# Kernel optimization log

Hardware: AMD Instinct MI355X
Metric: run time of the kernel (lower is better)

The kernel has to match this reference:

```python
import jax, jax.numpy as jnp
import numpy as np

D_MODEL = 1024
D_STATE = 16
DT_RANK = 64  # ceil(1024/16)
DT_MIN, DT_MAX = 1e-3, 1e-1


def setup_inputs() -> dict:
    key = jax.random.key(0)
    ks = jax.random.split(key, 6)
    x = jax.random.normal(ks[0], (2, 2048, D_MODEL), jnp.float32)
    A_log = jax.random.normal(ks[1], (D_MODEL, D_STATE), jnp.float32)
    D = jax.random.normal(ks[2], (D_MODEL,), jnp.float32)
    # nn.Linear default init ~ U(-1/sqrt(fan_in), 1/sqrt(fan_in)); normal*scale is fine for a baseline
    x_proj_w = jax.random.normal(ks[3], (DT_RANK + 2 * D_STATE, D_MODEL), jnp.float32) * (D_MODEL ** -0.5)
    dt_init_std = DT_RANK ** -0.5
    dt_proj_w = jax.random.uniform(ks[4], (D_MODEL, DT_RANK), jnp.float32, -dt_init_std, dt_init_std)
    dt = jnp.exp(jax.random.uniform(ks[5], (D_MODEL,), jnp.float32)
                 * (np.log(DT_MAX) - np.log(DT_MIN)) + np.log(DT_MIN))
    dt_proj_b = dt + jnp.log(-jnp.expm1(-dt))  # inverse-softplus init
    return {"x": x, "A_log": A_log, "D": D, "x_proj_w": x_proj_w,
            "dt_proj_w": dt_proj_w, "dt_proj_b": dt_proj_b}


def _s6(x, A_log, D, x_proj_w, dt_proj_w, dt_proj_b):
    A = -jnp.exp(A_log)                                    # (d, n)
    xp = jnp.einsum('bld,ed->ble', x, x_proj_w)            # (b, l, r+2n)
    d_rank = xp[..., :DT_RANK]
    Bm = xp[..., DT_RANK:DT_RANK + D_STATE]                # (b, l, n)
    Cm = xp[..., DT_RANK + D_STATE:]                       # (b, l, n)
    delta = jax.nn.softplus(jnp.einsum('blr,dr->bld', d_rank, dt_proj_w) + dt_proj_b)
    deltaA = jnp.exp(jnp.einsum('bld,dn->bldn', delta, A))          # (b, l, d, n)
    deltaB_u = jnp.einsum('bld,bln,bld->bldn', delta, Bm, x)        # (b, l, d, n)

    def step(h, inp):
        dA_t, dBu_t, C_t = inp          # (b,d,n), (b,d,n), (b,n)
        h = dA_t * h + dBu_t
        y = jnp.einsum('bdn,bn->bd', h, C_t)
        return h, y

    b, l, d = x.shape
    h0 = jnp.zeros((b, d, D_STATE), x.dtype)
    _, ys = jax.lax.scan(step, h0,
                         (deltaA.transpose(1, 0, 2, 3),
                          deltaB_u.transpose(1, 0, 2, 3),
                          Cm.transpose(1, 0, 2)))
    y = ys.transpose(1, 0, 2) + x * D                      # (b, l, d)
    return y


def reference(x, A_log, D, x_proj_w, dt_proj_w, dt_proj_b):
    return _s6(x, A_log, D, x_proj_w, dt_proj_w, dt_proj_b)
```

## Files before the change

### kernel.cpp

```cpp
#include <hip/hip_runtime.h>
#include <math.h>

#define Bb 2
#define Ll 2048
#define Dm 1024
#define Ns 16
#define Rr 64
#define Ee 96
#define XPS 8
#define BLK (Bb*Ll)
#define NTHR 256

__global__ void __launch_bounds__(NTHR)
k_xproj(const float* __restrict__ x, const float* __restrict__ xw,
        float* __restrict__ xp_part) {
    __shared__ float xs[64 * 37];
    __shared__ float wsh[96 * 37];
    int bx = blockIdx.x;
    int ks = bx & 7, mt = bx >> 3;
    int i0 = mt * 64;
    int tid = threadIdx.x;
    int tx = tid & 15, ty = tid >> 4;
    float acc[4][6];
#pragma unroll
    for (int ii = 0; ii < 4; ++ii)
#pragma unroll
        for (int jj = 0; jj < 6; ++jj) acc[ii][jj] = 0.f;

    for (int kc = 0; kc < 4; ++kc) {
        int k0 = ks * 128 + kc * 32;
        for (int t = tid; t < 512; t += NTHR) {
            int r = t >> 3, c = (t & 7) * 4;
            float4 v = *(const float4*)(x + (size_t)(i0 + r) * Dm + k0 + c);
            xs[r*37+c] = v.x; xs[r*37+c+1] = v.y; xs[r*37+c+2] = v.z; xs[r*37+c+3] = v.w;
        }
        for (int t = tid; t < 768; t += NTHR) {
            int r = t >> 3, c = (t & 7) * 4;
            float4 v = *(const float4*)(xw + (size_t)r * Dm + k0 + c);
            wsh[r*37+c] = v.x; wsh[r*37+c+1] = v.y; wsh[r*37+c+2] = v.z; wsh[r*37+c+3] = v.w;
        }
        __syncthreads();
#pragma unroll 8
        for (int k = 0; k < 32; ++k) {
            float xv[4], wv[6];
#pragma unroll
            for (int ii = 0; ii < 4; ++ii) xv[ii] = xs[(ty*4+ii)*37 + k];
#pragma unroll
            for (int jj = 0; jj < 6; ++jj) wv[jj] = wsh[(tx*6+jj)*37 + k];
#pragma unroll
            for (int ii = 0; ii < 4; ++ii)
#pragma unroll
                for (int jj = 0; jj < 6; ++jj)
                    acc[ii][jj] = fmaf(xv[ii], wv[jj], acc[ii][jj]);
        }
        __syncthreads();
    }
#pragma unroll
    for (int ii = 0; ii < 4; ++ii)
#pragma unroll
        for (int jj = 0; jj < 6; ++jj)
            xp_part[((size_t)ks * BLK + (i0 + ty*4 + ii)) * Ee + tx*6 + jj] = acc[ii][jj];
}

__global__ void __launch_bounds__(NTHR)
k_prep(const float* __restrict__ xp_part, float* __restrict__ xp) {
    int g = blockIdx.x * NTHR + threadIdx.x;
    const float4* p = (const float4*)xp_part;
    float4 s = p[g];
#pragma unroll
    for (int i = 1; i < XPS; ++i) {
        float4 v = p[(size_t)i * (BLK * Ee / 4) + g];
        s.x += v.x; s.y += v.y; s.z += v.z; s.w += v.w;
    }
    ((float4*)xp)[g] = s;
}

__global__ void __launch_bounds__(NTHR)
k_delta(const float* __restrict__ xp, const float* __restrict__ dtw,
        const float* __restrict__ dtb, float* __restrict__ delta) {
    __shared__ float xs[64 * 65];
    __shared__ float wsh[64 * 65];
    int bx = blockIdx.x;
    int nt = bx & 15, mt = bx >> 4;
    int i0 = mt * 64, j0 = nt * 64;
    int tid = threadIdx.x, tx = tid & 15, ty = tid >> 4;

    for (int t = tid; t < 1024; t += NTHR) {
        int r = t >> 4, c = (t & 15) * 4;
        float4 v = *(const float4*)(xp + (size_t)(i0 + r) * Ee + c);
        xs[r*65+c] = v.x; xs[r*65+c+1] = v.y; xs[r*65+c+2] = v.z; xs[r*65+c+3] = v.w;
        float4 w = *(const float4*)(dtw + (size_t)(j0 + r) * Rr + c);
        wsh[r*65+c] = w.x; wsh[r*65+c+1] = w.y; wsh[r*65+c+2] = w.z; wsh[r*65+c+3] = w.w;
    }
    __syncthreads();

    float acc[4][4];
#pragma unroll
    for (int ii = 0; ii < 4; ++ii)
#pragma unroll
        for (int jj = 0; jj < 4; ++jj) acc[ii][jj] = 0.f;
#pragma unroll 8
    for (int k = 0; k < 64; ++k) {
        float xv[4], wv[4];
#pragma unroll
        for (int ii = 0; ii < 4; ++ii) xv[ii] = xs[(ty*4+ii)*65 + k];
#pragma unroll
        for (int jj = 0; jj < 4; ++jj) wv[jj] = wsh[(tx*4+jj)*65 + k];
#pragma unroll
        for (int ii = 0; ii < 4; ++ii)
#pragma unroll
            for (int jj = 0; jj < 4; ++jj)
                acc[ii][jj] = fmaf(xv[ii], wv[jj], acc[ii][jj]);
    }
    int d0 = j0 + tx * 4;
    float4 bias = *(const float4*)(dtb + d0);
#pragma unroll
    for (int ii = 0; ii < 4; ++ii) {
        int bl = i0 + ty*4 + ii;
        float z0 = acc[ii][0] + bias.x, z1 = acc[ii][1] + bias.y;
        float z2 = acc[ii][2] + bias.z, z3 = acc[ii][3] + bias.w;
        float4 o;
        o.x = fmaxf(z0, 0.f) + log1pf(__expf(-fabsf(z0)));
        o.y = fmaxf(z1, 0.f) + log1pf(__expf(-fabsf(z1)));
        o.z = fmaxf(z2, 0.f) + log1pf(__expf(-fabsf(z2)));
        o.w = fmaxf(z3, 0.f) + log1pf(__expf(-fabsf(z3)));
        *(float4*)(delta + (size_t)bl * Dm + d0) = o;
    }
}

__device__ inline void load_a(const float* __restrict__ A_log, int d, float* a) {
    const float4* Ap = (const float4*)(A_log + (size_t)d * Ns);
    float4 a0 = Ap[0], a1 = Ap[1], a2 = Ap[2], a3 = Ap[3];
    float tmp[Ns] = {a0.x,a0.y,a0.z,a0.w, a1.x,a1.y,a1.z,a1.w,
                     a2.x,a2.y,a2.z,a2.w, a3.x,a3.y,a3.z,a3.w};
#pragma unroll
    for (int n = 0; n < Ns; ++n) a[n] = -__expf(tmp[n]);
}

template<int CHv>
__global__ void __launch_bounds__(NTHR)
k_scan_part(const float* __restrict__ delta, const float* __restrict__ x,
            const float* __restrict__ xp, const float* __restrict__ A_log,
            float* __restrict__ Ec, float* __restrict__ Sc) {
    constexpr int CLv = Ll / CHv;
    int bx = blockIdx.x;
    int dblk = bx & 3, chunk = (bx >> 2) & (CHv - 1), b = bx >> 2 >> __builtin_ctz(CHv);
    int tid = threadIdx.x;
    int d = dblk * 256 + tid;
    int row0 = b * Ll + chunk * CLv;

    float a[Ns], h[Ns];
    load_a(A_log, d, a);
#pragma unroll
    for (int n = 0; n < Ns; ++n) h[n] = 0.f;
    float sd = 0.f;

#pragma unroll 4
    for (int t = 0; t < CLv; ++t) {
        size_t row = (size_t)(row0 + t);
        float dl = delta[row * Dm + d];
        float xv = x[row * Dm + d];
        const float* bp = xp + row * Ee + Rr;
        float4 B0 = *(const float4*)(bp + 0),  B1 = *(const float4*)(bp + 4);
        float4 B2 = *(const float4*)(bp + 8),  B3 = *(const float4*)(bp + 12);
        float Bv[Ns] = {B0.x,B0.y,B0.z,B0.w, B1.x,B1.y,B1.z,B1.w,
                        B2.x,B2.y,B2.z,B2.w, B3.x,B3.y,B3.z,B3.w};
        float dx = dl * xv;
        sd += dl;
#pragma unroll
        for (int n = 0; n < Ns; ++n)
            h[n] = fmaf(__expf(dl * a[n]), h[n], dx * Bv[n]);
    }
    size_t base = ((size_t)b * CHv + chunk) * Dm + d;
    float4* Ep = (float4*)(Ec + base * Ns);
    Ep[0] = make_float4(h[0],  h[1],  h[2],  h[3]);
    Ep[1] = make_float4(h[4],  h[5],  h[6],  h[7]);
    Ep[2] = make_float4(h[8],  h[9],  h[10], h[11]);
    Ep[3] = make_float4(h[12], h[13], h[14], h[15]);
    Sc[base] = sd;
}

template<int CHv>
__global__ void __launch_bounds__(NTHR)
k_combine(const float* __restrict__ Ec, const float* __restrict__ Sc,
          const float* __restrict__ A_log, float* __restrict__ Hin) {
    int gid = blockIdx.x * NTHR + threadIdx.x;
    int n = gid & (Ns - 1);
    int d = (gid >> 4) & (Dm - 1);
    int b = gid >> 14;
    float a = -__expf(A_log[d * Ns + n]);
    float h = 0.f;
    for (int c = 0; c < CHv; ++c) {
        size_t base = ((size_t)b * CHv + c) * Dm + d;
        Hin[base * Ns + n] = h;
        float P = __expf(a * Sc[base]);
        h = fmaf(P, h, Ec[base * Ns + n]);
    }
}

template<int CHv>
__global__ void __launch_bounds__(NTHR)
k_scan_full(const float* __restrict__ delta, const float* __restrict__ x,
            const float* __restrict__ xp, const float* __restrict__ A_log,
            const float* __restrict__ Dp, const float* __restrict__ Hin,
            float* __restrict__ out) {
    constexpr int CLv = Ll / CHv;
    int bx = blockIdx.x;
    int dblk = bx & 3, chunk = (bx >> 2) & (CHv - 1), b = bx >> 2 >> __builtin_ctz(CHv);
    int tid = threadIdx.x;
    int d = dblk * 256 + tid;
    int row0 = b * Ll + chunk * CLv;

    float a[Ns], h[Ns];
    load_a(A_log, d, a);
    size_t base = ((size_t)b * CHv + chunk) * Dm + d;
    {
        const float4* Hp = (const float4*)(Hin + base * Ns);
        float4 h0 = Hp[0], h1 = Hp[1], h2 = Hp[2], h3 = Hp[3];
        h[0]=h0.x; h[1]=h0.y; h[2]=h0.z; h[3]=h0.w;
        h[4]=h1.x; h[5]=h1.y; h[6]=h1.z; h[7]=h1.w;
        h[8]=h2.x; h[9]=h2.y; h[10]=h2.z; h[11]=h2.w;
        h[12]=h3.x; h[13]=h3.y; h[14]=h3.z; h[15]=h3.w;
    }
    float Dval = Dp[d];

#pragma unroll 4
    for (int t = 0; t < CLv; ++t) {
        size_t row = (size_t)(row0 + t);
        float dl = delta[row * Dm + d];
        float xv = x[row * Dm + d];
        const float* bp = xp + row * Ee + Rr;
        float4 B0 = *(const float4*)(bp + 0),  B1 = *(const float4*)(bp + 4);
        float4 B2 = *(const float4*)(bp + 8),  B3 = *(const float4*)(bp + 12);
        float4 C0 = *(const float4*)(bp + 16), C1 = *(const float4*)(bp + 20);
        float4 C2 = *(const float4*)(bp + 24), C3 = *(const float4*)(bp + 28);
        float Bv[Ns] = {B0.x,B0.y,B0.z,B0.w, B1.x,B1.y,B1.z,B1.w,
                        B2.x,B2.y,B2.z,B2.w, B3.x,B3.y,B3.z,B3.w};
        float Cv[Ns] = {C0.x,C0.y,C0.z,C0.w, C1.x,C1.y,C1.z,C1.w,
                        C2.x,C2.y,C2.z,C2.w, C3.x,C3.y,C3.z,C3.w};
        float dx = dl * xv;
        float y = 0.f;
#pragma unroll
        for (int n = 0; n < Ns; ++n) {
            h[n] = fmaf(__expf(dl * a[n]), h[n], dx * Bv[n]);
            y = fmaf(h[n], Cv[n], y);
        }
        out[row * Dm + d] = fmaf(xv, Dval, y);
    }
}

extern "C" void kernel_launch(void* const* d_in, const int* in_sizes, int n_in,
                              void* d_out, int out_size, void* d_ws, size_t ws_size,
                              hipStream_t stream) {
    const float* x     = (const float*)d_in[0];
    const float* A_log = (const float*)d_in[1];
    const float* Dp    = (const float*)d_in[2];
    const float* xw    = (const float*)d_in[3];
    const float* dtw   = (const float*)d_in[4];
    const float* dtb   = (const float*)d_in[5];
    float* out = (float*)d_out;
    float* ws  = (float*)d_ws;

    float* xp      = ws;
    float* delta   = xp + 393216;
    float* S3      = delta + 4194304;
    float* xp_part = S3;

    k_xproj<<<dim3(512),  dim3(NTHR), 0, stream>>>(x, xw, xp_part);
    k_prep <<<dim3(384),  dim3(NTHR), 0, stream>>>(xp_part, xp);
    k_delta<<<dim3(1024), dim3(NTHR), 0, stream>>>(xp, dtw, dtb, delta);

    size_t need128 = (size_t)(393216 + 4194304 + 8650752) * 4;
    if (ws_size >= need128) {
        constexpr int CHv = 128;
        float* Ec  = S3;
        float* Sc  = Ec + (size_t)Bb*CHv*Dm*Ns;
        float* Hin = Sc + (size_t)Bb*CHv*Dm;
        k_scan_part<CHv><<<dim3(Bb*CHv*4), dim3(NTHR), 0, stream>>>(delta, x, xp, A_log, Ec, Sc);
        k_combine  <CHv><<<dim3(128),      dim3(NTHR), 0, stream>>>(Ec, Sc, A_log, Hin);
        k_scan_full<CHv><<<dim3(Bb*CHv*4), dim3(NTHR), 0, stream>>>(delta, x, xp, A_log, Dp, Hin, out);
    } else {
        constexpr int CHv = 64;
        float* Ec  = S3;
        float* Sc  = Ec + (size_t)Bb*CHv*Dm*Ns;
        float* Hin = Sc + (size_t)Bb*CHv*Dm;
        k_scan_part<CHv><<<dim3(Bb*CHv*4), dim3(NTHR), 0, stream>>>(delta, x, xp, A_log, Ec, Sc);
        k_combine  <CHv><<<dim3(128),      dim3(NTHR), 0, stream>>>(Ec, Sc, A_log, Hin);
        k_scan_full<CHv><<<dim3(Bb*CHv*4), dim3(NTHR), 0, stream>>>(delta, x, xp, A_log, Dp, Hin, out);
    }
}
```

Measured before the change: 165.0 us.

## Split chunk-combine into two-level scan, transpose GEMM smem tiles, use exp2

```diff
diff --git a/kernel.cpp b/kernel.cpp
--- a/kernel.cpp
+++ b/kernel.cpp
@@ -10,12 +10,33 @@
 #define XPS 8
 #define BLK (Bb*Ll)
 #define NTHR 256
+#define LOG2E 1.4426950408889634f
+#define LN2   0.6931471805599453f
+
+__device__ inline float ex2(float x) {
+#if __has_builtin(__builtin_amdgcn_exp2f)
+    return __builtin_amdgcn_exp2f(x);
+#else
+    return exp2f(x);
+#endif
+}
+__device__ inline float lg2(float x) {
+#if __has_builtin(__builtin_amdgcn_logf)
+    return __builtin_amdgcn_logf(x);
+#else
+    return log2f(x);
+#endif
+}
+__device__ inline float softplus_f(float z) {
+    float e = ex2(-fabsf(z) * LOG2E);
+    return fmaxf(z, 0.f) + lg2(1.f + e) * LN2;
+}
 
 __global__ void __launch_bounds__(NTHR)
 k_xproj(const float* __restrict__ x, const float* __restrict__ xw,
         float* __restrict__ xp_part) {
-    __shared__ float xs[64 * 37];
-    __shared__ float wsh[96 * 37];
+    __shared__ __align__(16) float xs[32 * 68];
+    __shared__ __align__(16) float wsh[32 * 100];
     int bx = blockIdx.x;
     int ks = bx & 7, mt = bx >> 3;
     int i0 = mt * 64;
@@ -32,26 +53,29 @@
         for (int t = tid; t < 512; t += NTHR) {
             int r = t >> 3, c = (t & 7) * 4;
             float4 v = *(const float4*)(x + (size_t)(i0 + r) * Dm + k0 + c);
-            xs[r*37+c] = v.x; xs[r*37+c+1] = v.y; xs[r*37+c+2] = v.z; xs[r*37+c+3] = v.w;
+            xs[(c+0)*68+r] = v.x; xs[(c+1)*68+r] = v.y;
+            xs[(c+2)*68+r] = v.z; xs[(c+3)*68+r] = v.w;
         }
         for (int t = tid; t < 768; t += NTHR) {
             int r = t >> 3, c = (t & 7) * 4;
             float4 v = *(const float4*)(xw + (size_t)r * Dm + k0 + c);
-            wsh[r*37+c] = v.x; wsh[r*37+c+1] = v.y; wsh[r*37+c+2] = v.z; wsh[r*37+c+3] = v.w;
+            wsh[(c+0)*100+r] = v.x; wsh[(c+1)*100+r] = v.y;
+            wsh[(c+2)*100+r] = v.z; wsh[(c+3)*100+r] = v.w;
         }
         __syncthreads();
 #pragma unroll 8
         for (int k = 0; k < 32; ++k) {
-            float xv[4], wv[6];
-#pragma unroll
-            for (int ii = 0; ii < 4; ++ii) xv[ii] = xs[(ty*4+ii)*37 + k];
-#pragma unroll
-            for (int jj = 0; jj < 6; ++jj) wv[jj] = wsh[(tx*6+jj)*37 + k];
+            float4 xv = *(const float4*)(xs + k*68 + ty*4);
+            float2 w0 = *(const float2*)(wsh + k*100 + tx*6 + 0);
+            float2 w1 = *(const float2*)(wsh + k*100 + tx*6 + 2);
+            float2 w2 = *(const float2*)(wsh + k*100 + tx*6 + 4);
+            float xr[4] = {xv.x, xv.y, xv.z, xv.w};
+            float wr[6] = {w0.x, w0.y, w1.x, w1.y, w2.x, w2.y};
 #pragma unroll
             for (int ii = 0; ii < 4; ++ii)
 #pragma unroll
                 for (int jj = 0; jj < 6; ++jj)
-                    acc[ii][jj] = fmaf(xv[ii], wv[jj], acc[ii][jj]);
+                    acc[ii][jj] = fmaf(xr[ii], wr[jj], acc[ii][jj]);
         }
         __syncthreads();
     }
@@ -78,63 +102,66 @@
 __global__ void __launch_bounds__(NTHR)
 k_delta(const float* __restrict__ xp, const float* __restrict__ dtw,
         const float* __restrict__ dtb, float* __restrict__ delta) {
-    __shared__ float xs[64 * 65];
-    __shared__ float wsh[64 * 65];
+    __shared__ __align__(16) float xs[64 * 136];
+    __shared__ __align__(16) float wsh[64 * 68];
     int bx = blockIdx.x;
     int nt = bx & 15, mt = bx >> 4;
-    int i0 = mt * 64, j0 = nt * 64;
+    int i0 = mt * 128, j0 = nt * 64;
     int tid = threadIdx.x, tx = tid & 15, ty = tid >> 4;
 
+    for (int t = tid; t < 2048; t += NTHR) {
+        int r = t >> 4, c = (t & 15) * 4;
+        float4 v = *(const float4*)(xp + (size_t)(i0 + r) * Ee + c);
+        xs[(c+0)*136+r] = v.x; xs[(c+1)*136+r] = v.y;
+        xs[(c+2)*136+r] = v.z; xs[(c+3)*136+r] = v.w;
+    }
     for (int t = tid; t < 1024; t += NTHR) {
         int r = t >> 4, c = (t & 15) * 4;
-        float4 v = *(const float4*)(xp + (size_t)(i0 + r) * Ee + c);
-        xs[r*65+c] = v.x; xs[r*65+c+1] = v.y; xs[r*65+c+2] = v.z; xs[r*65+c+3] = v.w;
         float4 w = *(const float4*)(dtw + (size_t)(j0 + r) * Rr + c);
-        wsh[r*65+c] = w.x; wsh[r*65+c+1] = w.y; wsh[r*65+c+2] = w.z; wsh[r*65+c+3] = w.w;
+        wsh[(c+0)*68+r] = w.x; wsh[(c+1)*68+r] = w.y;
+        wsh[(c+2)*68+r] = w.z; wsh[(c+3)*68+r] = w.w;
     }
     __syncthreads();
 
-    float acc[4][4];
-#pragma unroll
-    for (int ii = 0; ii < 4; ++ii)
+    float acc[8][4];
+#pragma unroll
+    for (int ii = 0; ii < 8; ++ii)
 #pragma unroll
         for (int jj = 0; jj < 4; ++jj) acc[ii][jj] = 0.f;
 #pragma unroll 8
     for (int k = 0; k < 64; ++k) {
-        float xv[4], wv[4];
-#pragma unroll
-        for (int ii = 0; ii < 4; ++ii) xv[ii] = xs[(ty*4+ii)*65 + k];
-#pragma unroll
-        for (int jj = 0; jj < 4; ++jj) wv[jj] = wsh[(tx*4+jj)*65 + k];
-#pragma unroll
-        for (int ii = 0; ii < 4; ++ii)
+        float4 xa = *(const float4*)(xs + k*136 + ty*8 + 0);
+        float4 xb = *(const float4*)(xs + k*136 + ty*8 + 4);
+        float4 wv = *(const float4*)(wsh + k*68 + tx*4);
+        float xr[8] = {xa.x,xa.y,xa.z,xa.w, xb.x,xb.y,xb.z,xb.w};
+        float wr[4] = {wv.x, wv.y, wv.z, wv.w};
+#pragma unroll
+        for (int ii = 0; ii < 8; ++ii)
 #pragma unroll
             for (int jj = 0; jj < 4; ++jj)
-                acc[ii][jj] = fmaf(xv[ii], wv[jj], acc[ii][jj]);
+                acc[ii][jj] = fmaf(xr[ii], wr[jj], acc[ii][jj]);
     }
     int d0 = j0 + tx * 4;
     float4 bias = *(const float4*)(dtb + d0);
 #pragma unroll
-    for (int ii = 0; ii < 4; ++ii) {
-        int bl = i0 + ty*4 + ii;
-        float z0 = acc[ii][0] + bias.x, z1 = acc[ii][1] + bias.y;
-        float z2 = acc[ii][2] + bias.z, z3 = acc[ii][3] + bias.w;
+    for (int ii = 0; ii < 8; ++ii) {
+        int bl = i0 + ty*8 + ii;
         float4 o;
-        o.x = fmaxf(z0, 0.f) + log1pf(__expf(-fabsf(z0)));
-        o.y = fmaxf(z1, 0.f) + log1pf(__expf(-fabsf(z1)));
-        o.z = fmaxf(z2, 0.f) + log1pf(__expf(-fabsf(z2)));
-        o.w = fmaxf(z3, 0.f) + log1pf(__expf(-fabsf(z3)));
+        o.x = softplus_f(acc[ii][0] + bias.x);
+        o.y = softplus_f(acc[ii][1] + bias.y);
+        o.z = softplus_f(acc[ii][2] + bias.z);
+        o.w = softplus_f(acc[ii][3] + bias.w);
         *(float4*)(delta + (size_t)bl * Dm + d0) = o;
     }
 }
 
-__device__ inline void load_a(const float* __restrict__ A_log, int d, float* a) {
+__device__ inline void load_a2(const float* __restrict__ A_log, int d, float* a2) {
     const float4* Ap = (const float4*)(A_log + (size_t)d * Ns);
-    float4 a0 = Ap[0], a1 = Ap[1], a2 = Ap[2], a3 = Ap[3];
+    float4 a0 = Ap[0], a1 = Ap[1], a2v = Ap[2], a3 = Ap[3];
     float tmp[Ns] = {a0.x,a0.y,a0.z,a0.w, a1.x,a1.y,a1.z,a1.w,
-                     a2.x,a2.y,a2.z,a2.w, a3.x,a3.y,a3.z,a3.w};
-#pragma unroll
-    for (int n = 0; n < Ns; ++n) a[n] = -__expf(tmp[n]);
+                     a2v.x,a2v.y,a2v.z,a2v.w, a3.x,a3.y,a3.z,a3.w};
+#pragma unroll
+    for (int n = 0; n < Ns; ++n) a2[n] = -__expf(tmp[n]) * LOG2E;
 }
 
 template<int CHv>
@@ -149,8 +176,8 @@
     int d = dblk * 256 + tid;
     int row0 = b * Ll + chunk * CLv;
 
-    float a[Ns], h[Ns];
-    load_a(A_log, d, a);
+    float a2[Ns], h[Ns];
+    load_a2(A_log, d, a2);
 #pragma unroll
     for (int n = 0; n < Ns; ++n) h[n] = 0.f;
     float sd = 0.f;
@@ -169,7 +196,7 @@
         sd += dl;
 #pragma unroll
         for (int n = 0; n < Ns; ++n)
-            h[n] = fmaf(__expf(dl * a[n]), h[n], dx * Bv[n]);
+            h[n] = fmaf(ex2(dl * a2[n]), h[n], dx * Bv[n]);
     }
     size_t base = ((size_t)b * CHv + chunk) * Dm + d;
     float4* Ep = (float4*)(Ec + base * Ns);
@@ -180,47 +207,83 @@
     Sc[base] = sd;
 }
 
-template<int CHv>
-__global__ void __launch_bounds__(NTHR)
-k_combine(const float* __restrict__ Ec, const float* __restrict__ Sc,
-          const float* __restrict__ A_log, float* __restrict__ Hin) {
+template<int CHv, int G>
+__global__ void __launch_bounds__(NTHR)
+k_comb1(const float* __restrict__ Ec, const float* __restrict__ Sc,
+        const float* __restrict__ A_log, float* __restrict__ Hloc,
+        float* __restrict__ Spre, float* __restrict__ Eg, float* __restrict__ Sg) {
+    constexpr int CPG = CHv / G;
+    int gid = blockIdx.x * NTHR + threadIdx.x;
+    int n = gid & (Ns - 1);
+    int d = (gid >> 4) & (Dm - 1);
+    int g = (gid >> 14) & (G - 1);
+    int b = gid >> 17;
+    float a2 = -__expf(A_log[d * Ns + n]) * LOG2E;
+    float h = 0.f, S = 0.f;
+#pragma unroll
+    for (int j = 0; j < CPG; ++j) {
+        size_t base = ((size_t)b * CHv + g * CPG + j) * Dm + d;
+        float e  = Ec[base * Ns + n];
+        float sc = Sc[base];
+        Hloc[base * Ns + n] = h;
+        if (n == 0) Spre[base] = S;
+        h = fmaf(ex2(a2 * sc), h, e);
+        S += sc;
+    }
+    size_t gb = ((size_t)b * G + g) * Dm + d;
+    Eg[gb * Ns + n] = h;
+    if (n == 0) Sg[gb] = S;
+}
+
+template<int G>
+__global__ void __launch_bounds__(NTHR)
+k_comb2(const float* __restrict__ Eg, const float* __restrict__ Sg,
+        const float* __restrict__ A_log, float* __restrict__ Hg) {
     int gid = blockIdx.x * NTHR + threadIdx.x;
     int n = gid & (Ns - 1);
     int d = (gid >> 4) & (Dm - 1);
     int b = gid >> 14;
-    float a = -__expf(A_log[d * Ns + n]);
+    float a2 = -__expf(A_log[d * Ns + n]) * LOG2E;
     float h = 0.f;
-    for (int c = 0; c < CHv; ++c) {
-        size_t base = ((size_t)b * CHv + c) * Dm + d;
-        Hin[base * Ns + n] = h;
-        float P = __expf(a * Sc[base]);
-        h = fmaf(P, h, Ec[base * Ns + n]);
-    }
-}
-
-template<int CHv>
+#pragma unroll
+    for (int g = 0; g < G; ++g) {
+        size_t gb = ((size_t)b * G + g) * Dm + d;
+        Hg[gb * Ns + n] = h;
+        h = fmaf(ex2(a2 * Sg[gb]), h, Eg[gb * Ns + n]);
+    }
+}
+
+template<int CHv, int G>
 __global__ void __launch_bounds__(NTHR)
 k_scan_full(const float* __restrict__ delta, const float* __restrict__ x,
             const float* __restrict__ xp, const float* __restrict__ A_log,
-            const float* __restrict__ Dp, const float* __restrict__ Hin,
+            const float* __restrict__ Dp, const float* __restrict__ Hloc,
+            const float* __restrict__ Spre, const float* __restrict__ Hg,
             float* __restrict__ out) {
     constexpr int CLv = Ll / CHv;
+    constexpr int CPG = CHv / G;
     int bx = blockIdx.x;
     int dblk = bx & 3, chunk = (bx >> 2) & (CHv - 1), b = bx >> 2 >> __builtin_ctz(CHv);
     int tid = threadIdx.x;
     int d = dblk * 256 + tid;
     int row0 = b * Ll + chunk * CLv;
 
-    float a[Ns], h[Ns];
-    load_a(A_log, d, a);
+    float a2[Ns], h[Ns];
+    load_a2(A_log, d, a2);
     size_t base = ((size_t)b * CHv + chunk) * Dm + d;
+    size_t gb   = ((size_t)b * G + chunk / CPG) * Dm + d;
     {
-        const float4* Hp = (const float4*)(Hin + base * Ns);
-        float4 h0 = Hp[0], h1 = Hp[1], h2 = Hp[2], h3 = Hp[3];
-        h[0]=h0.x; h[1]=h0.y; h[2]=h0.z; h[3]=h0.w;
-        h[4]=h1.x; h[5]=h1.y; h[6]=h1.z; h[7]=h1.w;
-        h[8]=h2.x; h[9]=h2.y; h[10]=h2.z; h[11]=h2.w;
-        h[12]=h3.x; h[13]=h3.y; h[14]=h3.z; h[15]=h3.w;
+        float sp = Spre[base];
+        const float4* Hl = (const float4*)(Hloc + base * Ns);
+        const float4* Hp = (const float4*)(Hg + gb * Ns);
+        float4 l0 = Hl[0], l1 = Hl[1], l2 = Hl[2], l3 = Hl[3];
+        float4 g0 = Hp[0], g1 = Hp[1], g2 = Hp[2], g3 = Hp[3];
+        float lv[Ns] = {l0.x,l0.y,l0.z,l0.w, l1.x,l1.y,l1.z,l1.w,
+                        l2.x,l2.y,l2.z,l2.w, l3.x,l3.y,l3.z,l3.w};
+        float gv[Ns] = {g0.x,g0.y,g0.z,g0.w, g1.x,g1.y,g1.z,g1.w,
+                        g2.x,g2.y,g2.z,g2.w, g3.x,g3.y,g3.z,g3.w};
+#pragma unroll
+        for (int n = 0; n < Ns; ++n) h[n] = fmaf(ex2(a2[n] * sp), gv[n], lv[n]);
     }
     float Dval = Dp[d];
 
@@ -239,13 +302,13 @@
         float Cv[Ns] = {C0.x,C0.y,C0.z,C0.w, C1.x,C1.y,C1.z,C1.w,
                         C2.x,C2.y,C2.z,C2.w, C3.x,C3.y,C3.z,C3.w};
         float dx = dl * xv;
-        float y = 0.f;
+        float ya[4] = {0.f, 0.f, 0.f, 0.f};
 #pragma unroll
         for (int n = 0; n < Ns; ++n) {
-            h[n] = fmaf(__expf(dl * a[n]), h[n], dx * Bv[n]);
-            y = fmaf(h[n], Cv[n], y);
+            h[n] = fmaf(ex2(dl * a2[n]), h[n], dx * Bv[n]);
+            ya[n & 3] = fmaf(h[n], Cv[n], ya[n & 3]);
         }
-        out[row * Dm + d] = fmaf(xv, Dval, y);
+        out[row * Dm + d] = fmaf(xv, Dval, (ya[0] + ya[1]) + (ya[2] + ya[3]));
     }
 }
 
@@ -266,26 +329,40 @@
     float* S3      = delta + 4194304;
     float* xp_part = S3;
 
-    k_xproj<<<dim3(512),  dim3(NTHR), 0, stream>>>(x, xw, xp_part);
-    k_prep <<<dim3(384),  dim3(NTHR), 0, stream>>>(xp_part, xp);
-    k_delta<<<dim3(1024), dim3(NTHR), 0, stream>>>(xp, dtw, dtb, delta);
-
-    size_t need128 = (size_t)(393216 + 4194304 + 8650752) * 4;
+    k_xproj<<<dim3(512), dim3(NTHR), 0, stream>>>(x, xw, xp_part);
+    k_prep <<<dim3(384), dim3(NTHR), 0, stream>>>(xp_part, xp);
+    k_delta<<<dim3(512), dim3(NTHR), 0, stream>>>(xp, dtw, dtb, delta);
+
+    constexpr int G = 8;
+    size_t s3_128 = (size_t)Bb*128*Dm*Ns + (size_t)Bb*128*Dm + (size_t)Bb*128*Dm*Ns
+                  + (size_t)Bb*128*Dm + (size_t)Bb*G*Dm*Ns + (size_t)Bb*G*Dm
+                  + (size_t)Bb*G*Dm*Ns;
+    size_t need128 = ((size_t)393216 + 4194304 + s3_128) * 4;
     if (ws_size >= need128) {
         constexpr int CHv = 128;
-        float* Ec  = S3;
-        float* Sc  = Ec + (size_t)Bb*CHv*Dm*Ns;
-        float* Hin = Sc + (size_t)Bb*CHv*Dm;
-        k_scan_part<CHv><<<dim3(Bb*CHv*4), dim3(NTHR), 0, stream>>>(delta, x, xp, A_log, Ec, Sc);
-        k_combine  <CHv><<<dim3(128),      dim3(NTHR), 0, stream>>>(Ec, Sc, A_log, Hin);
-        k_scan_full<CHv><<<dim3(Bb*CHv*4), dim3(NTHR), 0, stream>>>(delta, x, xp, A_log, Dp, Hin, out);
+        float* Ec   = S3;
+        float* Sc   = Ec   + (size_t)Bb*CHv*Dm*Ns;
+        float* Hloc = Sc   + (size_t)Bb*CHv*Dm;
+        float* Spre = Hloc + (size_t)Bb*CHv*Dm*Ns;
+        float* Eg   = Spre + (size_t)Bb*CHv*Dm;
+        float* Sg   = Eg   + (size_t)Bb*G*Dm*Ns;
+        float* Hg   = Sg   + (size_t)Bb*G*Dm;
+        k_scan_part<CHv>  <<<dim3(Bb*CHv*4), dim3(NTHR), 0, stream>>>(delta, x, xp, A_log, Ec, Sc);
+        k_comb1<CHv, G>   <<<dim3(Bb*G*Dm*Ns/NTHR), dim3(NTHR), 0, stream>>>(Ec, Sc, A_log, Hloc, Spre, Eg, Sg);
+        k_comb2<G>        <<<dim3(Bb*Dm*Ns/NTHR), dim3(NTHR), 0, stream>>>(Eg, Sg, A_log, Hg);
+        k_scan_full<CHv,G><<<dim3(Bb*CHv*4), dim3(NTHR), 0, stream>>>(delta, x, xp, A_log, Dp, Hloc, Spre, Hg, out);
     } else {
         constexpr int CHv = 64;
-        float* Ec  = S3;
-        float* Sc  = Ec + (size_t)Bb*CHv*Dm*Ns;
-        float* Hin = Sc + (size_t)Bb*CHv*Dm;
-        k_scan_part<CHv><<<dim3(Bb*CHv*4), dim3(NTHR), 0, stream>>>(delta, x, xp, A_log, Ec, Sc);
-        k_combine  <CHv><<<dim3(128),      dim3(NTHR), 0, stream>>>(Ec, Sc, A_log, Hin);
-        k_scan_full<CHv><<<dim3(Bb*CHv*4), dim3(NTHR), 0, stream>>>(delta, x, xp, A_log, Dp, Hin, out);
-    }
-}
+        float* Ec   = S3;
+        float* Sc   = Ec   + (size_t)Bb*CHv*Dm*Ns;
+        float* Hloc = Sc   + (size_t)Bb*CHv*Dm;
+        float* Spre = Hloc + (size_t)Bb*CHv*Dm*Ns;
+        float* Eg   = Spre + (size_t)Bb*CHv*Dm;
+        float* Sg   = Eg   + (size_t)Bb*G*Dm*Ns;
+        float* Hg   = Sg   + (size_t)Bb*G*Dm;
+        k_scan_part<CHv>  <<<dim3(Bb*CHv*4), dim3(NTHR), 0, stream>>>(delta, x, xp, A_log, Ec, Sc);
+        k_comb1<CHv, G>   <<<dim3(Bb*G*Dm*Ns/NTHR), dim3(NTHR), 0, stream>>>(Ec, Sc, A_log, Hloc, Spre, Eg, Sg);
+        k_comb2<G>        <<<dim3(Bb*Dm*Ns/NTHR), dim3(NTHR), 0, stream>>>(Eg, Sg, A_log, Hg);
+        k_scan_full<CHv,G><<<dim3(Bb*CHv*4), dim3(NTHR), 0, stream>>>(delta, x, xp, A_log, Dp, Hloc, Spre, Hg, out);
+    }
+}
```

New measurement: 152.3 us. 7.7% less time.
